# Performance work log

Hardware: AMD Instinct MI355X
Metric: run time of the kernel (lower is better)

## Reference

```python
import jax, jax.numpy as jnp
import numpy as np

TEMP = 0.07
EPS = 1e-8
NUM_CLASSES = 7
THRESH = 0.3


def setup_inputs() -> dict:
    key = jax.random.key(0)
    k1, k2, k3, k4, k5 = jax.random.split(key, 5)
    N, H, E, C = 8192, 128, 256, NUM_CLASSES
    reps = jax.random.normal(k1, (N, H), dtype=jnp.float32)
    labels = jax.random.randint(k2, (N,), 0, C, dtype=jnp.int64 if jax.config.jax_enable_x64 else jnp.int32)
    centers = jax.random.normal(k3, (C, E), dtype=jnp.float32)
    fc_w = jax.random.normal(k4, (H, E), dtype=jnp.float32) * (1.0 / np.sqrt(E))
    fc_b = jax.random.normal(k5, (H,), dtype=jnp.float32) * 0.01
    return {"reps": reps, "labels": labels, "centers": centers, "fc_w": fc_w, "fc_b": fc_b}


def reference(reps, labels, centers, fc_w, fc_b):
    # fc(default_centers): [C, H]
    curr_centers = centers @ fc_w.T + fc_b
    pad_labels = jnp.arange(NUM_CLASSES, dtype=labels.dtype)

    all_reps = jnp.concatenate([reps, curr_centers], axis=0)      # [M, H]
    all_labels = jnp.concatenate([labels, pad_labels], axis=0)    # [M]
    B = reps.shape[0]
    M = all_reps.shape[0]

    # cosine similarity via normalized matmul (avoids [B,M,H] broadcast)
    norms = jnp.sqrt(jnp.sum(all_reps * all_reps, axis=-1))
    rn = all_reps / jnp.maximum(norms, 1e-8)[:, None]
    cos = rn[:B] @ rn.T                                           # [B, M]

    scores = (1.0 + cos) * 0.5 + EPS
    eye = (jnp.arange(B)[:, None] == jnp.arange(M)[None, :]).astype(scores.dtype)
    scores = scores * (1.0 - eye) / TEMP
    # torch uses .item() on the max -> a non-differentiable constant
    scores = scores - jax.lax.stop_gradient(jnp.max(scores))
    e = jnp.exp(scores)

    pos_mask = (labels[:, None] == all_labels[None, :]).astype(scores.dtype)  # [B, M]
    mask = 1.0 - eye

    pos_sum = jnp.sum(e * pos_mask * mask, axis=-1)
    neg_sum = jnp.sum(e * (1.0 - pos_mask), axis=-1)
    probs = pos_sum / (pos_sum + neg_sum)
    probs = probs / (jnp.sum(pos_mask * mask, axis=-1) + EPS)

    loss_vec = -jnp.log(probs + EPS)
    loss_mask = (loss_vec > THRESH).astype(loss_vec.dtype)
    denom = jax.lax.stop_gradient(jnp.sum(loss_mask)) + EPS
    loss = jnp.sum(loss_vec * loss_mask) / denom
    return loss
```

## Files before the change

### kernel.cpp

```cpp
#include <hip/hip_runtime.h>
#include <hip/hip_bf16.h>

#define BN 8192
#define MM 8199
#define MP 8208
#define HH 128
#define EE 256
#define NTILE 513
#define JCH 32
#define K2 10.30496147f

typedef __attribute__((ext_vector_type(8))) short short8;
typedef __attribute__((ext_vector_type(4))) float floatx4;

__global__ __launch_bounds__(256)
void norm_kernel(const float* __restrict__ reps,
                 const float* __restrict__ centers,
                 const float* __restrict__ fc_w,
                 const float* __restrict__ fc_b,
                 const int* __restrict__ labels,
                 __hip_bfloat16* __restrict__ rn,
                 int* __restrict__ labp) {
  const int lane = threadIdx.x & 63;
  const int r = blockIdx.x * 4 + (threadIdx.x >> 6);
  float2 v = make_float2(0.f, 0.f);
  if (r < BN) {
    v = ((const float2*)(reps + (size_t)r * HH))[lane];
  } else if (r < MM) {
    int c = r - BN;
    const float4* ce = (const float4*)(centers + c * EE);
    const float4* w0 = (const float4*)(fc_w + (size_t)(2 * lane) * EE);
    const float4* w1 = (const float4*)(fc_w + (size_t)(2 * lane + 1) * EE);
    float s0 = 0.f, s1 = 0.f;
#pragma unroll 8
    for (int e = 0; e < 64; ++e) {
      float4 a = ce[e];
      float4 x = w0[e];
      float4 y = w1[e];
      s0 += a.x * x.x + a.y * x.y + a.z * x.z + a.w * x.w;
      s1 += a.x * y.x + a.y * y.y + a.z * y.z + a.w * y.w;
    }
    float2 bb = ((const float2*)fc_b)[lane];
    v.x = s0 + bb.x;
    v.y = s1 + bb.y;
  }
  float ss = v.x * v.x + v.y * v.y;
#pragma unroll
  for (int m = 1; m < 64; m <<= 1) ss += __shfl_xor(ss, m);
  float inv = 1.0f / fmaxf(sqrtf(ss), 1e-8f);
  __hip_bfloat162 h2;
  h2.x = __float2bfloat16(v.x * inv);
  h2.y = __float2bfloat16(v.y * inv);
  ((__hip_bfloat162*)(rn + (size_t)r * HH))[lane] = h2;
  if (lane == 0) labp[r] = (r < BN) ? labels[r] : (r < MM ? r - BN : -1);
}

__global__ __launch_bounds__(256, 4)
void main_kernel(const __hip_bfloat16* __restrict__ rn,
                 const int* __restrict__ labp,
                 float* __restrict__ tot,
                 float* __restrict__ pos) {
  const int tid = threadIdx.x;
  const int lane = tid & 63;
  const int wv = tid >> 6;
  const int q = lane >> 4, col = lane & 15;
  const int ibase = blockIdx.x * 128 + wv * 32;
  const short* rns = (const short*)rn;

  short8 afrag[2][4];
#pragma unroll
  for (int it = 0; it < 2; ++it) {
    const short8* p = (const short8*)(rns + (size_t)(ibase + it * 16 + col) * HH + q * 8);
    afrag[it][0] = p[0];
    afrag[it][1] = p[4];
    afrag[it][2] = p[8];
    afrag[it][3] = p[12];
  }
  int labi[2][4];
#pragma unroll
  for (int it = 0; it < 2; ++it)
#pragma unroll
    for (int r = 0; r < 4; ++r)
      labi[it][r] = labp[ibase + it * 16 + q * 4 + r];

  float stot[2][4] = {};
  float spos[2][4] = {};

  int t = blockIdx.y;
  const short8* bp = (const short8*)(rns + (size_t)(t * 16 + col) * HH + q * 8);
  short8 b0 = bp[0], b1 = bp[4], b2 = bp[8], b3 = bp[12];
  int labj = labp[t * 16 + col];

  while (t < NTILE) {
    const int tn = t + JCH;
    const int ts = (tn < NTILE) ? tn : t;
    const short8* np = (const short8*)(rns + (size_t)(ts * 16 + col) * HH + q * 8);
    short8 n0 = np[0], n1 = np[4], n2 = np[8], n3 = np[12];
    int labn = labp[ts * 16 + col];

    const int jb = t * 16;
#pragma unroll
    for (int it = 0; it < 2; ++it) {
      floatx4 acc = {0.f, 0.f, 0.f, 0.f};
      acc = __builtin_amdgcn_mfma_f32_16x16x32_bf16(afrag[it][0], b0, acc, 0, 0, 0);
      acc = __builtin_amdgcn_mfma_f32_16x16x32_bf16(afrag[it][1], b1, acc, 0, 0, 0);
      acc = __builtin_amdgcn_mfma_f32_16x16x32_bf16(afrag[it][2], b2, acc, 0, 0, 0);
      acc = __builtin_amdgcn_mfma_f32_16x16x32_bf16(afrag[it][3], b3, acc, 0, 0, 0);
      const bool isdiag = (jb == ibase + it * 16);
#pragma unroll
      for (int r = 0; r < 4; ++r) {
        float e = __builtin_amdgcn_exp2f(__builtin_fmaf(acc[r], K2, -K2));
        if (isdiag && (col == q * 4 + r)) e = 0.f;
        stot[it][r] += e;
        spos[it][r] += (labj == labi[it][r]) ? e : 0.f;
      }
    }
    b0 = n0; b1 = n1; b2 = n2; b3 = n3; labj = labn;
    t = tn;
  }

#pragma unroll
  for (int it = 0; it < 2; ++it)
#pragma unroll
    for (int r = 0; r < 4; ++r) {
      float tt = stot[it][r], pp = spos[it][r];
#pragma unroll
      for (int m = 1; m <= 8; m <<= 1) {
        tt += __shfl_xor(tt, m);
        pp += __shfl_xor(pp, m);
      }
      if (col == 0) {
        int i = ibase + it * 16 + q * 4 + r;
        atomicAdd(&tot[i], tt);
        atomicAdd(&pos[i], pp);
      }
    }
}

__global__ __launch_bounds__(1024)
void loss_kernel(const float* __restrict__ tot,
                 const float* __restrict__ pos,
                 const int* __restrict__ labels,
                 float* __restrict__ out) {
  __shared__ int hist[8];
  __shared__ float s1[1024], s2[1024];
  const int tid = threadIdx.x;
  if (tid < 8) hist[tid] = 0;
  __syncthreads();
  for (int i = tid; i < BN; i += 1024) atomicAdd(&hist[labels[i]], 1);
  __syncthreads();
  const float padc = 9.0f * exp2f(-K2);
  float lsum = 0.f, msum = 0.f;
  for (int i = tid; i < BN; i += 1024) {
    float t = tot[i] - padc, p = pos[i];
    float c = (float)hist[labels[i]];
    float pr = (p / t) / (c + 1e-8f);
    float lv = -logf(pr + 1e-8f);
    if (lv > 0.3f) { lsum += lv; msum += 1.f; }
  }
  s1[tid] = lsum; s2[tid] = msum;
  __syncthreads();
  for (int st = 512; st > 0; st >>= 1) {
    if (tid < st) { s1[tid] += s1[tid + st]; s2[tid] += s2[tid + st]; }
    __syncthreads();
  }
  if (tid == 0) out[0] = s1[0] / (s2[0] + 1e-8f);
}

extern "C" void kernel_launch(void* const* d_in, const int* in_sizes, int n_in,
                              void* d_out, int out_size, void* d_ws, size_t ws_size,
                              hipStream_t stream) {
  const float* reps    = (const float*)d_in[0];
  const int*   labels  = (const int*)d_in[1];
  const float* centers = (const float*)d_in[2];
  const float* fc_w    = (const float*)d_in[3];
  const float* fc_b    = (const float*)d_in[4];
  float* out = (float*)d_out;

  char* ws = (char*)d_ws;
  int* labp = (int*)ws;
  __hip_bfloat16* rn = (__hip_bfloat16*)(ws + 40960);
  float* tot = (float*)(ws + 40960 + 2101248);
  float* pos = tot + BN;

  hipMemsetAsync(tot, 0, 2 * BN * sizeof(float), stream);
  norm_kernel<<<MP / 4, 256, 0, stream>>>(reps, centers, fc_w, fc_b, labels, rn, labp);
  main_kernel<<<dim3(BN / 128, JCH), 256, 0, stream>>>(rn, labp, tot, pos);
  loss_kernel<<<1, 1024, 0, stream>>>(tot, pos, labels, out);
}
```

Baseline: 163.0 us.

## Use one-wave blocks with 64 rows, double-buffer B tiles, subtract diagonal analytically

The main kernel now runs single-wave blocks that each hold 64 A rows in registers, so every loaded B tile feeds more MFMAs. B tiles are double-buffered through two register sets in an unrolled loop. The per-element diagonal check is removed: norm_kernel stores the squared norm of each bf16-rounded row, and loss_kernel subtracts the self term exp2((ssq-1)*K2) from both sums. The loss kernel also switches to shuffle-based histogram and reductions; the cost is higher register pressure from 16 fragments and accumulators, and a slight numeric difference versus the in-loop masking.

New measurement: 146.4 us. -10.2%, faster.

```diff
diff --git a/kernel.cpp b/kernel.cpp
--- a/kernel.cpp
+++ b/kernel.cpp
@@ -20,7 +20,8 @@
                  const float* __restrict__ fc_b,
                  const int* __restrict__ labels,
                  __hip_bfloat16* __restrict__ rn,
-                 int* __restrict__ labp) {
+                 int* __restrict__ labp,
+                 float* __restrict__ ssq) {
   const int lane = threadIdx.x & 63;
   const int r = blockIdx.x * 4 + (threadIdx.x >> 6);
   float2 v = make_float2(0.f, 0.f);
@@ -52,75 +53,100 @@
   h2.x = __float2bfloat16(v.x * inv);
   h2.y = __float2bfloat16(v.y * inv);
   ((__hip_bfloat162*)(rn + (size_t)r * HH))[lane] = h2;
-  if (lane == 0) labp[r] = (r < BN) ? labels[r] : (r < MM ? r - BN : -1);
-}
-
-__global__ __launch_bounds__(256, 4)
+  float xr = __bfloat162float(h2.x);
+  float yr = __bfloat162float(h2.y);
+  float s2 = xr * xr + yr * yr;
+#pragma unroll
+  for (int m = 1; m < 64; m <<= 1) s2 += __shfl_xor(s2, m);
+  if (lane == 0) {
+    labp[r] = (r < BN) ? labels[r] : (r < MM ? r - BN : -1);
+    ssq[r] = s2;
+  }
+}
+
+__global__ __launch_bounds__(64)
 void main_kernel(const __hip_bfloat16* __restrict__ rn,
                  const int* __restrict__ labp,
                  float* __restrict__ tot,
                  float* __restrict__ pos) {
-  const int tid = threadIdx.x;
-  const int lane = tid & 63;
-  const int wv = tid >> 6;
+  const int lane = threadIdx.x;
   const int q = lane >> 4, col = lane & 15;
-  const int ibase = blockIdx.x * 128 + wv * 32;
+  const int ibase = blockIdx.x * 64;
   const short* rns = (const short*)rn;
 
-  short8 afrag[2][4];
-#pragma unroll
-  for (int it = 0; it < 2; ++it) {
+  short8 afrag[4][4];
+#pragma unroll
+  for (int it = 0; it < 4; ++it) {
     const short8* p = (const short8*)(rns + (size_t)(ibase + it * 16 + col) * HH + q * 8);
     afrag[it][0] = p[0];
     afrag[it][1] = p[4];
     afrag[it][2] = p[8];
     afrag[it][3] = p[12];
   }
-  int labi[2][4];
-#pragma unroll
-  for (int it = 0; it < 2; ++it)
+  int labi[4][4];
+#pragma unroll
+  for (int it = 0; it < 4; ++it)
 #pragma unroll
     for (int r = 0; r < 4; ++r)
       labi[it][r] = labp[ibase + it * 16 + q * 4 + r];
 
-  float stot[2][4] = {};
-  float spos[2][4] = {};
+  float stot[4][4] = {};
+  float spos[4][4] = {};
+
+  short8 A0, A1, A2, A3, B0, B1, B2, B3;
+  int Al, Bl;
+
+#define LOADSET(R0, R1, R2, R3, RL, TT)                                          \
+  {                                                                              \
+    const short8* _p = (const short8*)(rns + (size_t)((TT) * 16 + col) * HH + q * 8); \
+    R0 = _p[0]; R1 = _p[4]; R2 = _p[8]; R3 = _p[12];                             \
+    RL = labp[(TT) * 16 + col];                                                  \
+  }
+
+#define COMPUTE(R0, R1, R2, R3, RL)                                              \
+  {                                                                              \
+    _Pragma("unroll")                                                            \
+    for (int it = 0; it < 4; ++it) {                                             \
+      floatx4 acc = {0.f, 0.f, 0.f, 0.f};                                        \
+      acc = __builtin_amdgcn_mfma_f32_16x16x32_bf16(afrag[it][0], R0, acc, 0, 0, 0); \
+      acc = __builtin_amdgcn_mfma_f32_16x16x32_bf16(afrag[it][1], R1, acc, 0, 0, 0); \
+      acc = __builtin_amdgcn_mfma_f32_16x16x32_bf16(afrag[it][2], R2, acc, 0, 0, 0); \
+      acc = __builtin_amdgcn_mfma_f32_16x16x32_bf16(afrag[it][3], R3, acc, 0, 0, 0); \
+      _Pragma("unroll")                                                          \
+      for (int r = 0; r < 4; ++r) {                                              \
+        float e = __builtin_amdgcn_exp2f(__builtin_fmaf(acc[r], K2, -K2));       \
+        stot[it][r] += e;                                                        \
+        spos[it][r] += (RL == labi[it][r]) ? e : 0.f;                            \
+      }                                                                          \
+    }                                                                            \
+  }
 
   int t = blockIdx.y;
-  const short8* bp = (const short8*)(rns + (size_t)(t * 16 + col) * HH + q * 8);
-  short8 b0 = bp[0], b1 = bp[4], b2 = bp[8], b3 = bp[12];
-  int labj = labp[t * 16 + col];
-
-  while (t < NTILE) {
-    const int tn = t + JCH;
-    const int ts = (tn < NTILE) ? tn : t;
-    const short8* np = (const short8*)(rns + (size_t)(ts * 16 + col) * HH + q * 8);
-    short8 n0 = np[0], n1 = np[4], n2 = np[8], n3 = np[12];
-    int labn = labp[ts * 16 + col];
-
-    const int jb = t * 16;
-#pragma unroll
-    for (int it = 0; it < 2; ++it) {
-      floatx4 acc = {0.f, 0.f, 0.f, 0.f};
-      acc = __builtin_amdgcn_mfma_f32_16x16x32_bf16(afrag[it][0], b0, acc, 0, 0, 0);
-      acc = __builtin_amdgcn_mfma_f32_16x16x32_bf16(afrag[it][1], b1, acc, 0, 0, 0);
-      acc = __builtin_amdgcn_mfma_f32_16x16x32_bf16(afrag[it][2], b2, acc, 0, 0, 0);
-      acc = __builtin_amdgcn_mfma_f32_16x16x32_bf16(afrag[it][3], b3, acc, 0, 0, 0);
-      const bool isdiag = (jb == ibase + it * 16);
-#pragma unroll
-      for (int r = 0; r < 4; ++r) {
-        float e = __builtin_amdgcn_exp2f(__builtin_fmaf(acc[r], K2, -K2));
-        if (isdiag && (col == q * 4 + r)) e = 0.f;
-        stot[it][r] += e;
-        spos[it][r] += (labj == labi[it][r]) ? e : 0.f;
-      }
-    }
-    b0 = n0; b1 = n1; b2 = n2; b3 = n3; labj = labn;
-    t = tn;
-  }
-
-#pragma unroll
-  for (int it = 0; it < 2; ++it)
+  LOADSET(A0, A1, A2, A3, Al, t);
+  {
+    int tb = t + JCH; if (tb > NTILE - 1) tb = NTILE - 1;
+    LOADSET(B0, B1, B2, B3, Bl, tb);
+  }
+  for (;;) {
+    COMPUTE(A0, A1, A2, A3, Al);
+    if (t + JCH >= NTILE) break;
+    {
+      int tn = t + 2 * JCH; if (tn > NTILE - 1) tn = NTILE - 1;
+      LOADSET(A0, A1, A2, A3, Al, tn);
+    }
+    COMPUTE(B0, B1, B2, B3, Bl);
+    t += 2 * JCH;
+    if (t >= NTILE) break;
+    {
+      int tn = t + JCH; if (tn > NTILE - 1) tn = NTILE - 1;
+      LOADSET(B0, B1, B2, B3, Bl, tn);
+    }
+  }
+#undef LOADSET
+#undef COMPUTE
+
+#pragma unroll
+  for (int it = 0; it < 4; ++it)
 #pragma unroll
     for (int r = 0; r < 4; ++r) {
       float tt = stot[it][r], pp = spos[it][r];
@@ -140,31 +166,59 @@
 __global__ __launch_bounds__(1024)
 void loss_kernel(const float* __restrict__ tot,
                  const float* __restrict__ pos,
+                 const float* __restrict__ ssq,
                  const int* __restrict__ labels,
                  float* __restrict__ out) {
-  __shared__ int hist[8];
-  __shared__ float s1[1024], s2[1024];
+  __shared__ float hist[7];
+  __shared__ float s1[16], s2[16];
   const int tid = threadIdx.x;
-  if (tid < 8) hist[tid] = 0;
+  const int lane = tid & 63, wv = tid >> 6;
+  if (tid < 7) hist[tid] = 0.f;
   __syncthreads();
-  for (int i = tid; i < BN; i += 1024) atomicAdd(&hist[labels[i]], 1);
+  float c0 = 0, c1 = 0, c2 = 0, c3 = 0, c4 = 0, c5 = 0, c6 = 0;
+  for (int i = tid; i < BN; i += 1024) {
+    int lab = labels[i];
+    c0 += (lab == 0); c1 += (lab == 1); c2 += (lab == 2); c3 += (lab == 3);
+    c4 += (lab == 4); c5 += (lab == 5); c6 += (lab == 6);
+  }
+  float cc[7] = {c0, c1, c2, c3, c4, c5, c6};
+#pragma unroll
+  for (int k = 0; k < 7; ++k) {
+    float v = cc[k];
+#pragma unroll
+    for (int m = 1; m < 64; m <<= 1) v += __shfl_xor(v, m);
+    if (lane == 0) atomicAdd(&hist[k], v);
+  }
   __syncthreads();
+  float h[7];
+#pragma unroll
+  for (int k = 0; k < 7; ++k) h[k] = hist[k];
   const float padc = 9.0f * exp2f(-K2);
   float lsum = 0.f, msum = 0.f;
   for (int i = tid; i < BN; i += 1024) {
-    float t = tot[i] - padc, p = pos[i];
-    float c = (float)hist[labels[i]];
-    float pr = (p / t) / (c + 1e-8f);
+    int lab = labels[i];
+    float ch = h[0];
+#pragma unroll
+    for (int k = 1; k < 7; ++k) ch = (lab == k) ? h[k] : ch;
+    float eii = exp2f((ssq[i] - 1.f) * K2);
+    float t = tot[i] - padc - eii;
+    float p = pos[i] - eii;
+    float pr = (p / t) / (ch + 1e-8f);
     float lv = -logf(pr + 1e-8f);
     if (lv > 0.3f) { lsum += lv; msum += 1.f; }
   }
-  s1[tid] = lsum; s2[tid] = msum;
+#pragma unroll
+  for (int m = 1; m < 64; m <<= 1) {
+    lsum += __shfl_xor(lsum, m);
+    msum += __shfl_xor(msum, m);
+  }
+  if (lane == 0) { s1[wv] = lsum; s2[wv] = msum; }
   __syncthreads();
-  for (int st = 512; st > 0; st >>= 1) {
-    if (tid < st) { s1[tid] += s1[tid + st]; s2[tid] += s2[tid + st]; }
-    __syncthreads();
-  }
-  if (tid == 0) out[0] = s1[0] / (s2[0] + 1e-8f);
+  if (tid == 0) {
+    float L = 0.f, M = 0.f;
+    for (int w = 0; w < 16; ++w) { L += s1[w]; M += s2[w]; }
+    out[0] = L / (M + 1e-8f);
+  }
 }
 
 extern "C" void kernel_launch(void* const* d_in, const int* in_sizes, int n_in,
@@ -178,13 +232,14 @@
   float* out = (float*)d_out;
 
   char* ws = (char*)d_ws;
-  int* labp = (int*)ws;
-  __hip_bfloat16* rn = (__hip_bfloat16*)(ws + 40960);
-  float* tot = (float*)(ws + 40960 + 2101248);
+  int* labp  = (int*)ws;
+  float* ssq = (float*)(ws + 36864);
+  __hip_bfloat16* rn = (__hip_bfloat16*)(ws + 73728);
+  float* tot = (float*)(ws + 73728 + 2101248);
   float* pos = tot + BN;
 
   hipMemsetAsync(tot, 0, 2 * BN * sizeof(float), stream);
-  norm_kernel<<<MP / 4, 256, 0, stream>>>(reps, centers, fc_w, fc_b, labels, rn, labp);
-  main_kernel<<<dim3(BN / 128, JCH), 256, 0, stream>>>(rn, labp, tot, pos);
-  loss_kernel<<<1, 1024, 0, stream>>>(tot, pos, labels, out);
-}
+  norm_kernel<<<MP / 4, 256, 0, stream>>>(reps, centers, fc_w, fc_b, labels, rn, labp, ssq);
+  main_kernel<<<dim3(BN / 64, JCH), 64, 0, stream>>>(rn, labp, tot, pos);
+  loss_kernel<<<1, 1024, 0, stream>>>(tot, pos, ssq, labels, out);
+}
```
